# Optimization experiments

Hardware: AMD Instinct MI355X
Metric: run time of the kernel (lower is better)

## Reference

```python
import jax, jax.numpy as jnp
import numpy as np

B, C, H, W = 32, 256, 56, 56
NUM_ITER = 5

# Row-major upper-triangular (incl. diagonal) flat indices, matching
# torch.ones(C, C).triu().view(-1).nonzero() in the original triuvec.
_r, _c = np.triu_indices(C)
TRIU_IDX = jnp.asarray(_r * C + _c)


def setup_inputs() -> dict:
    key = jax.random.key(0)
    x = jax.random.normal(key, (B, C, H, W), dtype=jnp.float32)
    return {"x": x}


def _cov_pool(x):
    # x: (b, c, h, w) -> sigma = x_n @ ((1/n) I - (1/n^2) J) @ x_n^T : (b, c, c)
    b, c, h, w = x.shape
    n = h * w
    xn = x.reshape(b, c, n)
    s = xn.sum(axis=2)  # (b, c) = x_n @ ones
    gram = jnp.einsum('bcn,bdn->bcd', xn, xn)  # (b, c, c)
    return gram / n - jnp.einsum('bc,bd->bcd', s, s) / (n * n)


def _newton_schulz_sqrt(x, num_iter):
    # x: (b, m, m) SPD; returns approx matrix square root, scaled by sqrt(trace).
    b, m, _ = x.shape
    eye = jnp.eye(m, dtype=x.dtype)
    x_trace = jnp.trace(x, axis1=1, axis2=2)[:, None, None]  # (b, 1, 1)
    a = x / x_trace
    i3 = 3.0 * eye  # broadcasts over batch
    # iteration 0
    b2 = 0.5 * (i3 - a)
    yi = a @ b2
    zi = b2

    def body(carry, _):
        yi, zi = carry
        b2 = 0.5 * (i3 - zi @ yi)
        return (yi @ b2, b2 @ zi), None

    (yi, zi), _ = jax.lax.scan(body, (yi, zi), None, length=num_iter - 1)
    return yi * jnp.sqrt(x_trace)


def _triuvec(x):
    # (b, c, c) -> (b, c*(c+1)//2), row-major upper triangle incl. diagonal
    b, c, _ = x.shape
    return x.reshape(b, c * c)[:, TRIU_IDX]


def reference(x) -> jnp.ndarray:
    cov = _cov_pool(x)
    y = _newton_schulz_sqrt(cov, NUM_ITER)
    return _triuvec(y)
```

## Files before the change

### kernel.cpp

```cpp
#include <hip/hip_runtime.h>
#include <hip/hip_bf16.h>
#include <math.h>

#define BATCH 32
#define C 256
#define HW 3136
#define OUTROW 32896
#define KSPLIT 7
#define KCHUNK 448
#define KC32 98
#define G7 14
#define SLAB 16384
#define HALF 8192


typedef __bf16 b8v __attribute__((ext_vector_type(8)));
typedef float  f4v __attribute__((ext_vector_type(4)));
typedef unsigned short u16x8 __attribute__((ext_vector_type(8)));

__device__ __forceinline__ unsigned short f2bf(float f) {
    union { float f; unsigned u; } v; v.f = f;
    unsigned r = v.u + 0x7FFFu + ((v.u >> 16) & 1u);
    return (unsigned short)(r >> 16);
}
__device__ __forceinline__ float bf2f(unsigned short h) {
    union { unsigned u; float f; } v; v.u = ((unsigned)h) << 16; return v.f;
}
__device__ __forceinline__ void split2(float x, unsigned short& h, unsigned short& l) {
    h = f2bf(x);
    l = f2bf(x - bf2f(h));
}

__device__ __forceinline__ float wave_sum(float v) {
    for (int o = 32; o; o >>= 1) v += __shfl_down(v, o, 64);
    return v;
}

__global__ __launch_bounds__(256, 2) void k_prep(const float* __restrict__ x,
                                                 unsigned short* __restrict__ X,
                                                 float* __restrict__ psum,
                                                 float* __restrict__ qsum) {
    const int bid = blockIdx.x;
    const int quad = bid & 3;
    const int bg = bid >> 2;
    const int b = bg / G7;
    const int g = bg - b * G7;
    const int t = threadIdx.x;
    if (t >= 252) return;
    const int j = t % 7;
    const int rbase = t / 7;
    const int kc = g * 7 + j;

    const float* xb = x + (size_t)b * C * HW + (size_t)kc * 32;
    unsigned short* sl = X + (size_t)(b * KC32 + kc) * SLAB;
    float* ps = psum + ((size_t)b * KC32 + kc) * 256;
    float* qs = qsum + ((size_t)b * KC32 + kc) * 256;

#pragma unroll
    for (int p = 0; p < 2; ++p) {
        const int row = quad * 64 + p * 36 + rbase;
        if (row < quad * 64 + 64) {
            const float* src = xb + (size_t)row * HW;
            float4 v[8];
#pragma unroll
            for (int u = 0; u < 8; ++u) v[u] = *(const float4*)(src + u * 4);
            unsigned short h[32], l[32];
            float s = 0.f, q = 0.f;
#pragma unroll
            for (int u = 0; u < 8; ++u) {
                float f0 = v[u].x, f1 = v[u].y, f2 = v[u].z, f3 = v[u].w;
                split2(f0, h[u * 4 + 0], l[u * 4 + 0]);
                split2(f1, h[u * 4 + 1], l[u * 4 + 1]);
                split2(f2, h[u * 4 + 2], l[u * 4 + 2]);
                split2(f3, h[u * 4 + 3], l[u * 4 + 3]);
                s += f0 + f1 + f2 + f3;
                q = fmaf(f0, f0, q); q = fmaf(f1, f1, q);
                q = fmaf(f2, f2, q); q = fmaf(f3, f3, q);
            }
#pragma unroll
            for (int u = 0; u < 4; ++u) {
                *(u16x8*)(sl + (size_t)row * 32 + u * 8) = *(u16x8*)&h[u * 8];
                *(u16x8*)(sl + HALF + (size_t)row * 32 + u * 8) = *(u16x8*)&l[u * 8];
            }
            ps[row] = s;
            qs[row] = q;
        }
    }
}

__global__ __launch_bounds__(64, 1) void k_gram_split(
    const unsigned short* __restrict__ X, float* __restrict__ part) {
    const int bid = blockIdx.x;
    const int x8 = bid & 7;
    const int t8 = bid >> 3;
    const int pairIdx = t8 % 10;
    const int g = (t8 / 10) * 8 + x8;
    const int b = g & 31;
    const int z = g >> 5;

    int p = pairIdx, tm = 0, rem = 4;
    while (p >= rem) { p -= rem; ++tm; --rem; }
    const int tn = tm + p;

    const int lane = threadIdx.x & 63;
    const int q = lane >> 4, r = lane & 15;
    const int kc0 = z * (KCHUNK / 32);
    const size_t matb = (size_t)b * KC32 * SLAB;

    int oA[4], oB[4];
#pragma unroll
    for (int i = 0; i < 4; ++i) {
        oA[i] = (tm * 64 + i * 16 + r) * 32 + q * 8;
        oB[i] = (tn * 64 + i * 16 + r) * 32 + q * 8;
    }

    f4v acc[4][4] = {};
    b8v fAh[2][4], fAl[2][4], fBh[2][4], fBl[2][4];
#define LDG(buf, kc)                                                     \
    do {                                                                 \
        const size_t sb = matb + (size_t)(kc0 + (kc)) * SLAB;            \
        for (int i = 0; i < 4; ++i) {                                    \
            fAh[buf][i] = *(const b8v*)(X + sb + oA[i]);                 \
            fAl[buf][i] = *(const b8v*)(X + sb + HALF + oA[i]);          \
            fBh[buf][i] = *(const b8v*)(X + sb + oB[i]);                 \
            fBl[buf][i] = *(const b8v*)(X + sb + HALF + oB[i]);          \
        }                                                                \
    } while (0)

    LDG(0, 0);
#pragma unroll
    for (int kc = 0; kc < KCHUNK / 32; ++kc) {
        const int cb = kc & 1, nb = cb ^ 1;
        if (kc < KCHUNK / 32 - 1) LDG(nb, kc + 1);
#pragma unroll
        for (int i = 0; i < 4; ++i)
#pragma unroll
            for (int j = 0; j < 4; ++j) {
                acc[i][j] = __builtin_amdgcn_mfma_f32_16x16x32_bf16(fAh[cb][i], fBh[cb][j], acc[i][j], 0, 0, 0);
                acc[i][j] = __builtin_amdgcn_mfma_f32_16x16x32_bf16(fAh[cb][i], fBl[cb][j], acc[i][j], 0, 0, 0);
                acc[i][j] = __builtin_amdgcn_mfma_f32_16x16x32_bf16(fAl[cb][i], fBh[cb][j], acc[i][j], 0, 0, 0);
            }
    }
#undef LDG

    float* pt = part + (((size_t)pairIdx * BATCH + b) * KSPLIT + z) * 4096;
#pragma unroll
    for (int i = 0; i < 4; ++i)
#pragma unroll
        for (int j = 0; j < 4; ++j)
#pragma unroll
            for (int reg = 0; reg < 4; ++reg) {
                int row = i * 16 + q * 4 + reg;
                int col = j * 16 + r;
                pt[row * 64 + col] = acc[i][j][reg];
            }
}

__global__ __launch_bounds__(256) void k_reduce(
    const float* __restrict__ part, const float* __restrict__ psum,
    const float* __restrict__ qsum,
    unsigned short* __restrict__ A, unsigned short* __restrict__ Z,
    float* __restrict__ strbuf) {
    const int b = blockIdx.y;
    int p = blockIdx.x, tm = 0, rem = 4;
    while (p >= rem) { p -= rem; ++tm; --rem; }
    const int tn = tm + p;
    const int t = threadIdx.x;

    const float* ps = psum + (size_t)b * KC32 * 256 + t;
    const float* qs = qsum + (size_t)b * KC32 * 256 + t;
    float s0 = 0.f, q0 = 0.f;
#pragma unroll 7
    for (int kc = 0; kc < KC32; ++kc) {
        s0 += ps[(size_t)kc * 256];
        q0 += qs[(size_t)kc * 256];
    }
    __shared__ float ssum[256];
    __shared__ float red[4];
    ssum[t] = s0;
    const float invn = 1.f / (float)HW, invn2 = invn * invn;
    float v = q0 * invn - s0 * s0 * invn2;
    v = wave_sum(v);
    if ((t & 63) == 0) red[t >> 6] = v;
    __syncthreads();
    const float tr = red[0] + red[1] + red[2] + red[3];
    if (blockIdx.x == 0 && t == 0) strbuf[b] = sqrtf(tr);

    const float* pb = part + ((size_t)blockIdx.x * BATCH + b) * KSPLIT * 4096;
    const int row = t >> 2, c0 = (t & 3) * 16;

    float s[16];
#pragma unroll
    for (int u = 0; u < 16; ++u) s[u] = 0.f;
    for (int sp = 0; sp < KSPLIT; ++sp) {
        const float* q4 = pb + sp * 4096 + row * 64 + c0;
#pragma unroll
        for (int u4 = 0; u4 < 4; ++u4) {
            float4 w = *(const float4*)(q4 + u4 * 4);
            s[u4 * 4 + 0] += w.x; s[u4 * 4 + 1] += w.y;
            s[u4 * 4 + 2] += w.z; s[u4 * 4 + 3] += w.w;
        }
    }

    const int gi = tm * 64 + row;
    const float si = ssum[gi];
    const size_t mb = (size_t)b * 8 * SLAB;

    __shared__ unsigned short tAh[64][66], tAl[64][66], tZh[64][66], tZl[64][66];
    unsigned short vAh[16], vAl[16], vZh[16], vZl[16];
#pragma unroll
    for (int u = 0; u < 16; ++u) {
        int gj = tn * 64 + c0 + u;
        float sj = ssum[gj];
        float a = (s[u] * invn - si * sj * invn2) / tr;
        split2(a, vAh[u], vAl[u]);
        float zv = ((gi == gj) ? 1.5f : 0.f) - 0.5f * a;
        split2(zv, vZh[u], vZl[u]);
        tAh[row][c0 + u] = vAh[u]; tAl[row][c0 + u] = vAl[u];
        tZh[row][c0 + u] = vZh[u]; tZl[row][c0 + u] = vZl[u];
    }
#pragma unroll
    for (int u4 = 0; u4 < 4; ++u4) {
        const int col0 = tn * 64 + c0 + u4 * 4;
        const size_t off = mb + (size_t)(col0 >> 5) * SLAB + (size_t)gi * 32 + (col0 & 31);
        *(ushort4*)&A[off] = *(ushort4*)&vAh[u4 * 4];
        *(ushort4*)&A[off + HALF] = *(ushort4*)&vAl[u4 * 4];
        *(ushort4*)&Z[off] = *(ushort4*)&vZh[u4 * 4];
        *(ushort4*)&Z[off + HALF] = *(ushort4*)&vZl[u4 * 4];
    }
    if (tm != tn) {
        __syncthreads();
        const int mr = t >> 2, mc0 = (t & 3) * 16;
        const int gim = tn * 64 + mr;
        unsigned short wAh[16], wAl[16], wZh[16], wZl[16];
#pragma unroll
        for (int u = 0; u < 16; ++u) {
            wAh[u] = tAh[mc0 + u][mr]; wAl[u] = tAl[mc0 + u][mr];
            wZh[u] = tZh[mc0 + u][mr]; wZl[u] = tZl[mc0 + u][mr];
        }
#pragma unroll
        for (int u4 = 0; u4 < 4; ++u4) {
            const int col0 = tm * 64 + mc0 + u4 * 4;
            const size_t off = mb + (size_t)(col0 >> 5) * SLAB + (size_t)gim * 32 + (col0 & 31);
            *(ushort4*)&A[off] = *(ushort4*)&wAh[u4 * 4];
            *(ushort4*)&A[off + HALF] = *(ushort4*)&wAl[u4 * 4];
            *(ushort4*)&Z[off] = *(ushort4*)&wZh[u4 * 4];
            *(ushort4*)&Z[off + HALF] = *(ushort4*)&wZl[u4 * 4];
        }
    }
}

__device__ __forceinline__ void wave_gemm32(
    const unsigned short* __restrict__ A, const unsigned short* __restrict__ B,
    int rowA, int rowB, f4v acc[2][2]) {
    const int lane = threadIdx.x & 63;
    const int q = lane >> 4, r = lane & 15;
    int oA[2], oB[2];
#pragma unroll
    for (int i = 0; i < 2; ++i) {
        oA[i] = (rowA + i * 16 + r) * 32 + q * 8;
        oB[i] = (rowB + i * 16 + r) * 32 + q * 8;
    }
    b8v fAh[2][2], fAl[2][2], fBh[2][2], fBl[2][2];
#define LD(buf, kc)                                              \
    do {                                                         \
        const size_t sb = (size_t)(kc) * SLAB;                   \
        for (int i = 0; i < 2; ++i) {                            \
            fAh[buf][i] = *(const b8v*)(A + sb + oA[i]);         \
            fAl[buf][i] = *(const b8v*)(A + sb + HALF + oA[i]);  \
            fBh[buf][i] = *(const b8v*)(B + sb + oB[i]);         \
            fBl[buf][i] = *(const b8v*)(B + sb + HALF + oB[i]);  \
        }                                                        \
    } while (0)

    LD(0, 0);
#pragma unroll
    for (int kc = 0; kc < 8; ++kc) {
        const int cb = kc & 1, nb = cb ^ 1;
        if (kc < 7) LD(nb, kc + 1);
#pragma unroll
        for (int i = 0; i < 2; ++i)
#pragma unroll
            for (int j = 0; j < 2; ++j) {
                acc[i][j] = __builtin_amdgcn_mfma_f32_16x16x32_bf16(fAh[cb][i], fBh[cb][j], acc[i][j], 0, 0, 0);
                acc[i][j] = __builtin_amdgcn_mfma_f32_16x16x32_bf16(fAh[cb][i], fBl[cb][j], acc[i][j], 0, 0, 0);
                acc[i][j] = __builtin_amdgcn_mfma_f32_16x16x32_bf16(fAl[cb][i], fBh[cb][j], acc[i][j], 0, 0, 0);
            }
    }
#undef LD
}

__device__ __forceinline__ void store_tile32(
    unsigned short* __restrict__ D, int tm, int tn, const f4v acc[2][2], bool modeT) {
    const int lane = threadIdx.x & 63, q = lane >> 4, r = lane & 15;
#pragma unroll
    for (int i = 0; i < 2; ++i)
#pragma unroll
        for (int j = 0; j < 2; ++j) {
            const int gj = tn * 32 + j * 16 + r;
            const size_t cbase = (size_t)(gj >> 5) * SLAB + (gj & 31);
#pragma unroll
            for (int reg = 0; reg < 4; ++reg) {
                const int gi = tm * 32 + i * 16 + q * 4 + reg;
                float v = acc[i][j][reg];
                if (modeT) v = ((gi == gj) ? 1.5f : 0.f) - 0.5f * v;
                unsigned short h, l;
                split2(v, h, l);
                D[cbase + (size_t)gi * 32] = h;
                D[cbase + HALF + (size_t)gi * 32] = l;
            }
        }
}

template <int MODE>
__global__ __launch_bounds__(64, 1) void k_t64(
    const unsigned short* __restrict__ A, const unsigned short* __restrict__ B,
    unsigned short* __restrict__ D, float* __restrict__ outF,
    const float* __restrict__ strbuf) {
    const int bid = blockIdx.x;
    const int x8 = bid & 7;
    const int w = bid >> 3;
    int b, tm = 0, tn = 0;
    if (MODE == 2) {
        b = x8 + 8 * (w / 36);
        int p = w % 36, rem = 8;
        while (p >= rem) { p -= rem; ++tm; --rem; }
        tn = tm + p;
    } else {
        b = x8 + 8 * (w >> 6);
        const int tile = w & 63;
        tm = tile >> 3; tn = tile & 7;
    }
    const size_t mo = (size_t)b * 8 * SLAB;
    f4v acc[2][2] = {};
    wave_gemm32(A + mo, B + mo, tm * 32, tn * 32, acc);

    if (MODE == 2) {
        const int lane = threadIdx.x & 63, q = lane >> 4, r = lane & 15;
        const float sc = strbuf[b];
#pragma unroll
        for (int i = 0; i < 2; ++i)
#pragma unroll
            for (int j = 0; j < 2; ++j) {
                const int gj = tn * 32 + j * 16 + r;
#pragma unroll
                for (int reg = 0; reg < 4; ++reg) {
                    const int gi = tm * 32 + i * 16 + q * 4 + reg;
                    if (gj >= gi)
                        outF[(size_t)b * OUTROW + (size_t)(gi * C - (gi * (gi - 1)) / 2) +
                             (gj - gi)] = acc[i][j][reg] * sc;
                }
            }
    } else {
        store_tile32(D + mo, tm, tn, acc, MODE == 1);
    }
}

__global__ __launch_bounds__(64, 1) void k_yz64(
    const unsigned short* __restrict__ Y, const unsigned short* __restrict__ T,
    const unsigned short* __restrict__ Z,
    unsigned short* __restrict__ Yn, unsigned short* __restrict__ Zn) {
    const int bid = blockIdx.x;
    const int x8 = bid & 7;
    const int w = bid >> 3;
    const int zz = w >> 8;
    const int ww = w & 255;
    const int b = x8 + 8 * (ww >> 6);
    const int tile = ww & 63;
    const int tm = tile >> 3, tn = tile & 7;

    const unsigned short* Am = zz ? T : Y;
    const unsigned short* Bm = zz ? Z : T;
    unsigned short* Dm = zz ? Zn : Yn;

    const size_t mo = (size_t)b * 8 * SLAB;
    f4v acc[2][2] = {};
    wave_gemm32(Am + mo, Bm + mo, tm * 32, tn * 32, acc);
    store_tile32(Dm + mo, tm, tn, acc, false);
}

extern "C" void kernel_launch(void* const* d_in, const int* in_sizes, int n_in,
                              void* d_out, int out_size, void* d_ws, size_t ws_size,
                              hipStream_t stream) {
    const float* x = (const float*)d_in[0];
    float* out = (float*)d_out;

    unsigned short* W = (unsigned short*)d_ws;
    const size_t XS = (size_t)BATCH * KC32 * SLAB;
    const size_t MS = (size_t)BATCH * 8 * SLAB;
    unsigned short* X = W;
    float* strbuf = (float*)(X + XS);
    unsigned short* P = (unsigned short*)(strbuf + BATCH);
    unsigned short* PA = P + 0 * MS;
    unsigned short* PB = P + 1 * MS;
    unsigned short* PC = P + 2 * MS;
    unsigned short* PD = P + 3 * MS;
    unsigned short* PE = P + 4 * MS;
    float* part = (float*)PC;
    unsigned short* partEnd = PC + (size_t)2 * 10 * BATCH * KSPLIT * 4096;
    float* psum = (float*)partEnd;
    float* qsum = psum + (size_t)BATCH * KC32 * 256;

    k_prep<<<dim3(BATCH * G7 * 4), 256, 0, stream>>>(x, X, psum, qsum);
    k_gram_split<<<dim3(10 * BATCH * KSPLIT), 64, 0, stream>>>(X, part);
    k_reduce<<<dim3(10, BATCH), 256, 0, stream>>>(part, psum, qsum, PA, PB, strbuf);

    dim3 g2048(2048);
    k_t64<0><<<g2048, 64, 0, stream>>>(PA, PB, PC, nullptr, strbuf);
    k_t64<1><<<g2048, 64, 0, stream>>>(PB, PC, PD, nullptr, strbuf);
    k_yz64<<<dim3(4096), 64, 0, stream>>>(PC, PD, PB, PA, PE);
    k_t64<1><<<g2048, 64, 0, stream>>>(PE, PA, PB, nullptr, strbuf);
    k_yz64<<<dim3(4096), 64, 0, stream>>>(PA, PB, PE, PC, PD);
    k_t64<1><<<g2048, 64, 0, stream>>>(PD, PC, PA, nullptr, strbuf);
    k_yz64<<<dim3(4096), 64, 0, stream>>>(PC, PA, PD, PB, PE);
    k_t64<1><<<g2048, 64, 0, stream>>>(PE, PB, PC, nullptr, strbuf);
    k_t64<2><<<dim3(1152), 64, 0, stream>>>(PB, PC, nullptr, out, strbuf);
}
```

Baseline: 362.1 us.

## Stage bf16 split in LDS for coalesced stores and pre-reduce row sums

k_prep now writes the hi/lo bf16 splits into padded shared memory, then has all threads write out coalesced 16-byte chunks per K-chunk slab instead of scattered per-thread row writes. Row sum and sum-of-squares partials are reduced across the 7 K-chunks in the block, shrinking psum/qsum from 98 to 14 entries per batch and shortening k_reduce's loop. The cost is about 64KB of LDS per block, which limits occupancy, plus an extra barrier. Thread mapping changes from 252 to 224 active loaders.

```diff
diff --git a/kernel.cpp b/kernel.cpp
--- a/kernel.cpp
+++ b/kernel.cpp
@@ -12,6 +12,7 @@
 #define G7 14
 #define SLAB 16384
 #define HALF 8192
+#define LKС 0
 
 
 typedef __bf16 b8v __attribute__((ext_vector_type(8)));
@@ -36,6 +37,7 @@
     return v;
 }
 
+#define KCSTRIDE 2308
 __global__ __launch_bounds__(256, 2) void k_prep(const float* __restrict__ x,
                                                  unsigned short* __restrict__ X,
                                                  float* __restrict__ psum,
@@ -46,45 +48,69 @@
     const int b = bg / G7;
     const int g = bg - b * G7;
     const int t = threadIdx.x;
-    if (t >= 252) return;
+
+    __shared__ unsigned short lh[7 * KCSTRIDE];
+    __shared__ unsigned short ll[7 * KCSTRIDE];
+    __shared__ float ssq[2][7][64];
+
+    const bool act = t < 224;
     const int j = t % 7;
-    const int rbase = t / 7;
+    const int r32 = t / 7;
     const int kc = g * 7 + j;
 
-    const float* xb = x + (size_t)b * C * HW + (size_t)kc * 32;
-    unsigned short* sl = X + (size_t)(b * KC32 + kc) * SLAB;
-    float* ps = psum + ((size_t)b * KC32 + kc) * 256;
-    float* qs = qsum + ((size_t)b * KC32 + kc) * 256;
-
-#pragma unroll
-    for (int p = 0; p < 2; ++p) {
-        const int row = quad * 64 + p * 36 + rbase;
-        if (row < quad * 64 + 64) {
+    if (act) {
+        const float* xb = x + (size_t)b * C * HW + (size_t)(quad * 64) * HW + (size_t)kc * 32;
+#pragma unroll
+        for (int p = 0; p < 2; ++p) {
+            const int row = p * 32 + r32;
             const float* src = xb + (size_t)row * HW;
             float4 v[8];
 #pragma unroll
             for (int u = 0; u < 8; ++u) v[u] = *(const float4*)(src + u * 4);
-            unsigned short h[32], l[32];
+            unsigned short* lhr = lh + j * KCSTRIDE + row * 36;
+            unsigned short* llr = ll + j * KCSTRIDE + row * 36;
             float s = 0.f, q = 0.f;
 #pragma unroll
             for (int u = 0; u < 8; ++u) {
-                float f0 = v[u].x, f1 = v[u].y, f2 = v[u].z, f3 = v[u].w;
-                split2(f0, h[u * 4 + 0], l[u * 4 + 0]);
-                split2(f1, h[u * 4 + 1], l[u * 4 + 1]);
-                split2(f2, h[u * 4 + 2], l[u * 4 + 2]);
-                split2(f3, h[u * 4 + 3], l[u * 4 + 3]);
-                s += f0 + f1 + f2 + f3;
-                q = fmaf(f0, f0, q); q = fmaf(f1, f1, q);
-                q = fmaf(f2, f2, q); q = fmaf(f3, f3, q);
-            }
-#pragma unroll
-            for (int u = 0; u < 4; ++u) {
-                *(u16x8*)(sl + (size_t)row * 32 + u * 8) = *(u16x8*)&h[u * 8];
-                *(u16x8*)(sl + HALF + (size_t)row * 32 + u * 8) = *(u16x8*)&l[u * 8];
-            }
-            ps[row] = s;
-            qs[row] = q;
+                ushort4 h4, l4;
+                split2(v[u].x, h4.x, l4.x); split2(v[u].y, h4.y, l4.y);
+                split2(v[u].z, h4.z, l4.z); split2(v[u].w, h4.w, l4.w);
+                *(ushort4*)(lhr + u * 4) = h4;
+                *(ushort4*)(llr + u * 4) = l4;
+                s += v[u].x + v[u].y + v[u].z + v[u].w;
+                q = fmaf(v[u].x, v[u].x, q); q = fmaf(v[u].y, v[u].y, q);
+                q = fmaf(v[u].z, v[u].z, q); q = fmaf(v[u].w, v[u].w, q);
+            }
+            ssq[0][j][row] = s;
+            ssq[1][j][row] = q;
         }
+    }
+    __syncthreads();
+
+    const int wrow = t >> 2;
+    const int wo = (t & 3) * 8;
+#pragma unroll
+    for (int kcw = 0; kcw < 7; ++kcw) {
+        unsigned short* dst = X + (size_t)(b * KC32 + g * 7 + kcw) * SLAB +
+                              (size_t)(quad * 64 + wrow) * 32 + wo;
+        const unsigned short* sh = lh + kcw * KCSTRIDE + wrow * 36 + wo;
+        const unsigned short* sl = ll + kcw * KCSTRIDE + wrow * 36 + wo;
+        union { ushort4 u4[2]; u16x8 u8; } hv, lv;
+        hv.u4[0] = *(const ushort4*)(sh);
+        hv.u4[1] = *(const ushort4*)(sh + 4);
+        lv.u4[0] = *(const ushort4*)(sl);
+        lv.u4[1] = *(const ushort4*)(sl + 4);
+        *(u16x8*)dst = hv.u8;
+        *(u16x8*)(dst + HALF) = lv.u8;
+    }
+
+    if (t < 64) {
+        float s = 0.f, q = 0.f;
+#pragma unroll
+        for (int k7 = 0; k7 < 7; ++k7) { s += ssq[0][k7][t]; q += ssq[1][k7][t]; }
+        const size_t o = ((size_t)b * G7 + g) * 256 + quad * 64 + t;
+        psum[o] = s;
+        qsum[o] = q;
     }
 }
 
@@ -167,13 +193,13 @@
     const int tn = tm + p;
     const int t = threadIdx.x;
 
-    const float* ps = psum + (size_t)b * KC32 * 256 + t;
-    const float* qs = qsum + (size_t)b * KC32 * 256 + t;
+    const float* ps = psum + (size_t)b * G7 * 256 + t;
+    const float* qs = qsum + (size_t)b * G7 * 256 + t;
     float s0 = 0.f, q0 = 0.f;
-#pragma unroll 7
-    for (int kc = 0; kc < KC32; ++kc) {
-        s0 += ps[(size_t)kc * 256];
-        q0 += qs[(size_t)kc * 256];
+#pragma unroll
+    for (int g = 0; g < G7; ++g) {
+        s0 += ps[(size_t)g * 256];
+        q0 += qs[(size_t)g * 256];
     }
     __shared__ float ssum[256];
     __shared__ float red[4];
@@ -399,7 +425,7 @@
     float* part = (float*)PC;
     unsigned short* partEnd = PC + (size_t)2 * 10 * BATCH * KSPLIT * 4096;
     float* psum = (float*)partEnd;
-    float* qsum = psum + (size_t)BATCH * KC32 * 256;
+    float* qsum = psum + (size_t)BATCH * G7 * 256;
 
     k_prep<<<dim3(BATCH * G7 * 4), 256, 0, stream>>>(x, X, psum, qsum);
     k_gram_split<<<dim3(10 * BATCH * KSPLIT), 64, 0, stream>>>(X, part);
```

New measurement: 339.8 us. 1.07x faster.
